# Optimization experiments

Measured on AMD Instinct MI355X. Metric: run time of the kernel, lower is better.

Reference implementation:

```python
import jax, jax.numpy as jnp
import numpy as np

# Spec constants (from init_kwargs)
NUM_ANCHORS = 5
NUM_CLASSES = 80
FM_H = 19
FM_W = 19
MAX_OBJECT = 50
NOOBJECT_SCALE = 1.0
OBJECT_SCALE = 5.0
BACKGROUND_THRESHOLD = 0.6
COORD_SCALE = 1.0
CLASS_SCALE = 1.0


def _iou_cwh(a, b):
    """IoU for boxes in (cx, cy, w, h) format; broadcasts over leading dims.
    Matches bbox_iou(..., x1y1x2y2=False) in the torch repo (0 when no overlap)."""
    ax1, ax2 = a[..., 0] - a[..., 2] * 0.5, a[..., 0] + a[..., 2] * 0.5
    ay1, ay2 = a[..., 1] - a[..., 3] * 0.5, a[..., 1] + a[..., 3] * 0.5
    bx1, bx2 = b[..., 0] - b[..., 2] * 0.5, b[..., 0] + b[..., 2] * 0.5
    by1, by2 = b[..., 1] - b[..., 3] * 0.5, b[..., 1] + b[..., 3] * 0.5
    uw = jnp.maximum(ax2, bx2) - jnp.minimum(ax1, bx1)
    uh = jnp.maximum(ay2, by2) - jnp.minimum(ay1, by1)
    cw = a[..., 2] + b[..., 2] - uw
    ch = a[..., 3] + b[..., 3] - uh
    inter = jnp.where((cw > 0) & (ch > 0), cw * ch, 0.0)
    union = a[..., 2] * a[..., 3] + b[..., 2] * b[..., 3] - inter
    return inter / jnp.maximum(union, 1e-12)


def setup_inputs() -> dict:
    key = jax.random.key(0)
    k1, k2, k3, k4, k5 = jax.random.split(key, 5)
    B, A, C, H, W, T = 64, NUM_ANCHORS, NUM_CLASSES, FM_H, FM_W, MAX_OBJECT
    output = jax.random.normal(k1, (B, A * (5 + C), H, W), jnp.float32) * 0.5
    # targets: per object (class, cx, cy, w, h), normalized to [0,1]; list ends at first cx == 0
    cls_t = jax.random.randint(k2, (B, T), 0, C).astype(jnp.float32)
    xy = jax.random.uniform(k3, (B, T, 2), jnp.float32, minval=0.1, maxval=0.9)
    wh = jax.random.uniform(k4, (B, T, 2), jnp.float32, minval=0.05, maxval=0.4)
    nvalid = jax.random.randint(k5, (B,), 1, T + 1)
    valid = (jnp.arange(T)[None, :] < nvalid[:, None]).astype(jnp.float32)
    tgt = jnp.concatenate([cls_t[..., None], xy, wh], axis=-1) * valid[..., None]
    target = tgt.reshape(B, T * 5)
    anchors = jnp.array([[1.3221, 1.73145], [3.19275, 4.00944], [5.05587, 8.09892],
                         [9.47112, 4.84053], [11.2364, 10.0071]], jnp.float32)
    return {"output": output, "target": target, "anchors": anchors}


def reference(output, target, anchors):
    B = output.shape[0]
    A, C, H, W, T = NUM_ANCHORS, NUM_CLASSES, FM_H, FM_W, MAX_OBJECT
    out = output.reshape(B, A, 5 + C, H, W)
    x = jax.nn.sigmoid(out[:, :, 0])
    y = jax.nn.sigmoid(out[:, :, 1])
    w = out[:, :, 2]
    h = out[:, :, 3]
    conf = jax.nn.sigmoid(out[:, :, 4])
    cls_logits = jnp.transpose(out[:, :, 5:], (0, 1, 3, 4, 2))  # [B,A,H,W,C]

    # decoded predicted boxes in grid units (detached for target building, as in torch)
    px = x + jnp.arange(W, dtype=x.dtype)[None, None, None, :]
    py = y + jnp.arange(H, dtype=x.dtype)[None, None, :, None]
    pw = jnp.exp(w) * anchors[None, :, 0, None, None]
    ph = jnp.exp(h) * anchors[None, :, 1, None, None]
    pred = jax.lax.stop_gradient(jnp.stack([px, py, pw, ph], axis=-1))  # [B,A,H,W,4]

    tgt = target.reshape(B, T, 5)
    cls_t = tgt[..., 0]
    gx = tgt[..., 1] * W
    gy = tgt[..., 2] * H
    gw = tgt[..., 3] * W
    gh = tgt[..., 4] * H
    # break-at-first-zero semantics of the torch loop
    valid = jnp.cumprod((tgt[..., 1] != 0).astype(jnp.int32), axis=1).astype(bool)  # [B,T]

    gt_boxes = jnp.stack([gx, gy, gw, gh], axis=-1)  # [B,T,4]
    # all-pairs pred-vs-gt IoU (replaces per-object python loop)
    pred_flat = pred.reshape(B, A * H * W, 4)
    ious = _iou_cwh(pred_flat[:, :, None, :], gt_boxes[:, None, :, :])  # [B,N,T]
    best_iou = jnp.max(jnp.where(valid[:, None, :], ious, 0.0), axis=-1)  # [B,N]
    conf_mask = jnp.where(best_iou > BACKGROUND_THRESHOLD, 0.0, NOOBJECT_SCALE)
    conf_mask = conf_mask.reshape(B, A, H, W)

    # best anchor per gt: IoU of (w,h) boxes centered at origin
    aw = anchors[:, 0][None, None, :]
    ah = anchors[:, 1][None, None, :]
    inter_a = jnp.minimum(gw[..., None], aw) * jnp.minimum(gh[..., None], ah)
    union_a = gw[..., None] * gh[..., None] + aw * ah - inter_a
    best_n = jnp.argmax(inter_a / jnp.maximum(union_a, 1e-12), axis=-1)  # [B,T]

    gi = jnp.clip(gx.astype(jnp.int32), 0, W - 1)
    gj = jnp.clip(gy.astype(jnp.int32), 0, H - 1)
    bidx = jnp.arange(B)[:, None]
    pred_sel = pred[bidx, best_n, gj, gi]  # [B,T,4]
    iou_obj = _iou_cwh(gt_boxes, pred_sel)  # [B,T]

    N = B * A * H * W
    flat = ((bidx * A + best_n) * H + gj) * W + gi  # [B,T]
    flat = jnp.where(valid, flat, N).reshape(-1)  # invalid -> out of range, dropped

    def scat(vals):
        return jnp.zeros((N,), jnp.float32).at[flat].set(
            vals.reshape(-1), mode="drop").reshape(B, A, H, W)

    coord_mask = scat(jnp.ones_like(gx))
    cls_mask = coord_mask
    conf_mask = conf_mask.reshape(-1).at[flat].set(
        jnp.full((B * T,), OBJECT_SCALE, jnp.float32), mode="drop").reshape(B, A, H, W)
    tx = scat(gx - gi.astype(gx.dtype))
    ty = scat(gy - gj.astype(gy.dtype))
    tw = scat(jnp.log(jnp.maximum(gw, 1e-12) / anchors[best_n, 0]))
    th = scat(jnp.log(jnp.maximum(gh, 1e-12) / anchors[best_n, 1]))
    tconf = scat(iou_obj)
    tcls = scat(cls_t)

    # losses (sum reduction, matching MSELoss/CrossEntropyLoss(size_average=False))
    loss_x = COORD_SCALE * jnp.sum((coord_mask * (x - tx)) ** 2) / 2.0
    loss_y = COORD_SCALE * jnp.sum((coord_mask * (y - ty)) ** 2) / 2.0
    loss_w = COORD_SCALE * jnp.sum((coord_mask * (w - tw)) ** 2) / 2.0
    loss_h = COORD_SCALE * jnp.sum((coord_mask * (h - th)) ** 2) / 2.0
    sq = jnp.sqrt(conf_mask)
    loss_conf = jnp.sum((sq * (conf - tconf)) ** 2) / 2.0
    ce = -jnp.take_along_axis(jax.nn.log_softmax(cls_logits, axis=-1),
                              tcls.astype(jnp.int32)[..., None], axis=-1)[..., 0]
    loss_cls = CLASS_SCALE * jnp.sum(cls_mask * ce)
    return loss_x + loss_y + loss_w + loss_h + loss_conf + loss_cls
```

## Files before the change

kernel.cpp:

```cpp
#include <hip/hip_runtime.h>
#include <math.h>

#define NUM_ANCHORS 5
#define NUM_CLASSES 80
#define FM_H 19
#define FM_W 19
#define MAX_OBJECT 50
#define HW (FM_H * FM_W)
#define CELLS_PER_B (NUM_ANCHORS * HW)
#define CH (5 + NUM_CLASSES)
#define THREADS 512
#define NW (THREADS / 64)
#define BLOCKS_PER_B ((CELLS_PER_B + THREADS - 1) / THREADS)
#define OBJECT_SCALE 5.0f
#define BACKGROUND_THRESHOLD 0.6f

__device__ inline float frcp(float v) { return __builtin_amdgcn_rcpf(v); }
__device__ inline float fsigmoid(float v) { return frcp(1.0f + __expf(-v)); }

__global__ __launch_bounds__(THREADS) void yolov2_main(
    const float* __restrict__ out,
    const float* __restrict__ target,
    const float* __restrict__ anchors,
    float* __restrict__ partial)
{
    const int b    = blockIdx.x / BLOCKS_PER_B;
    const int blk  = blockIdx.x % BLOCKS_PER_B;
    const int cell = blk * THREADS + threadIdx.x;
    const int lane = threadIdx.x & 63;
    const int wid  = threadIdx.x >> 6;

    __shared__ float4 gA[MAX_OBJECT];
    __shared__ float4 gB[MAX_OBJECT];
    __shared__ float4 gT[MAX_OBJECT];
    __shared__ int    gcls[MAX_OBJECT];
    __shared__ int    nv_sh, n_obj;
    __shared__ int    entries[MAX_OBJECT];
    __shared__ float  wsum[NW];

    const bool incell = (cell < CELLS_PER_B);
    const int a    = incell ? (cell / HW) : 0;
    const int hw   = cell - a * HW;
    const int hrow = hw / FM_W;
    const int wcol = hw - hrow * FM_W;

    const float* base = out + ((size_t)(b * NUM_ANCHORS + a) * CH) * HW + hw;
    float ox = 0.f, oy = 0.f, ow = 0.f, oh = 0.f, oc = 0.f;
    if (incell) {
        ox = base[0];
        oy = base[HW];
        ow = base[2 * HW];
        oh = base[3 * HW];
        oc = base[4 * HW];
    }
    const float anc_w = anchors[2 * a];
    const float anc_h = anchors[2 * a + 1];

    if (threadIdx.x == 0) n_obj = 0;

    if (threadIdx.x < 64) {
        const int t = threadIdx.x;
        float f0 = 0.f, f1 = 0.f, f2 = 0.f, f3 = 0.f, f4 = 0.f;
        if (t < MAX_OBJECT) {
            const float* tp = target + (size_t)b * MAX_OBJECT * 5 + t * 5;
            f0 = tp[0]; f1 = tp[1]; f2 = tp[2]; f3 = tp[3]; f4 = tp[4];
        }
        unsigned long long m = __ballot(t < MAX_OBJECT && f1 != 0.0f);
        if (t == 0) nv_sh = __popcll(m);
        if (t < MAX_OBJECT) {
            float gx = f1 * (float)FM_W;
            float gy = f2 * (float)FM_H;
            float gw = f3 * (float)FM_W;
            float gh = f4 * (float)FM_H;
            int bn = 0; float best = -1.0f;
            #pragma unroll
            for (int k = 0; k < NUM_ANCHORS; ++k) {
                float aw = anchors[2 * k], ah = anchors[2 * k + 1];
                float inter = fminf(gw, aw) * fminf(gh, ah);
                float uni = gw * gh + aw * ah - inter;
                float r = inter * frcp(fmaxf(uni, 1e-12f));
                if (r > best) { best = r; bn = k; }
            }
            int gi = (int)gx; gi = gi < 0 ? 0 : (gi > FM_W - 1 ? FM_W - 1 : gi);
            int gj = (int)gy; gj = gj < 0 ? 0 : (gj > FM_H - 1 ? FM_H - 1 : gj);
            int acell = bn * HW + gj * FM_W + gi;
            gA[t] = make_float4(gx - gw * 0.5f, gx + gw * 0.5f,
                                gy - gh * 0.5f, gy + gh * 0.5f);
            gB[t] = make_float4(gw, gh, gw * gh, __int_as_float(acell));
            gT[t] = make_float4(gx - (float)gi, gy - (float)gj,
                                __logf(fmaxf(gw, 1e-12f) * frcp(anchors[2 * bn])),
                                __logf(fmaxf(gh, 1e-12f) * frcp(anchors[2 * bn + 1])));
            gcls[t] = (int)f0;
        }
    }
    __syncthreads();

    const int nv = nv_sh;
    float local = 0.0f;

    if (incell) {
        float x    = fsigmoid(ox);
        float y    = fsigmoid(oy);
        float conf = fsigmoid(oc);
        float px = x + (float)wcol;
        float py = y + (float)hrow;
        float pw = __expf(ow) * anc_w;
        float ph = __expf(oh) * anc_h;
        float ax1 = px - pw * 0.5f, ax2 = px + pw * 0.5f;
        float ay1 = py - ph * 0.5f, ay2 = py + ph * 0.5f;
        float parea = pw * ph;

        bool bg_hit = false;
        int  last_t = -1;
        #pragma unroll 5
        for (int t = 0; t < nv; ++t) {
            float4 A  = gA[t];
            float4 Bv = gB[t];
            float uw = fmaxf(ax2, A.y) - fminf(ax1, A.x);
            float uh = fmaxf(ay2, A.w) - fminf(ay1, A.z);
            float cw  = Bv.x + pw - uw;
            float chh = Bv.y + ph - uh;
            float inter = (cw > 0.f && chh > 0.f) ? cw * chh : 0.f;
            float uni = parea + Bv.z - inter;
            bg_hit = bg_hit || (inter > BACKGROUND_THRESHOLD * uni);
            if (__float_as_int(Bv.w) == cell) last_t = t;
        }

        if (last_t >= 0) {
            float4 A  = gA[last_t];
            float4 Bv = gB[last_t];
            float4 Tt = gT[last_t];
            float uw = fmaxf(ax2, A.y) - fminf(ax1, A.x);
            float uh = fmaxf(ay2, A.w) - fminf(ay1, A.z);
            float cw  = Bv.x + pw - uw;
            float chh = Bv.y + ph - uh;
            float inter = (cw > 0.f && chh > 0.f) ? cw * chh : 0.f;
            float tconf = inter * frcp(fmaxf(parea + Bv.z - inter, 1e-12f));
            float dc = conf - tconf; local += 0.5f * OBJECT_SCALE * dc * dc;
            float dx = x  - Tt.x; local += 0.5f * dx * dx;
            float dy = y  - Tt.y; local += 0.5f * dy * dy;
            float dw = ow - Tt.z; local += 0.5f * dw * dw;
            float dh = oh - Tt.w; local += 0.5f * dh * dh;
            int pos = atomicAdd(&n_obj, 1);
            entries[pos] = cell | (gcls[last_t] << 16);
        } else if (!bg_hit) {
            local += 0.5f * conf * conf;
        }
    }
    __syncthreads();

    const int ne = n_obj;
    const bool ld = (lane < NUM_CLASSES / 2);
    for (int e0 = wid; e0 < ne; e0 += 2 * NW) {
        const int eB = e0 + NW;
        const bool hasB = (eB < ne);

        int pkA    = entries[e0];
        int ecellA = pkA & 0xFFFF;
        int eclsA  = pkA >> 16;
        int eaA  = ecellA / HW;
        const float* clA = out + ((size_t)(b * NUM_ANCHORS + eaA) * CH + 5) * HW
                               + (ecellA - eaA * HW);
        float vA0 = ld ? clA[(2 * lane + 0) * HW] : 0.0f;
        float vA1 = ld ? clA[(2 * lane + 1) * HW] : 0.0f;

        float vB0 = 0.0f, vB1 = 0.0f;
        int eclsB = 0;
        if (hasB) {
            int pkB    = entries[eB];
            int ecellB = pkB & 0xFFFF;
            eclsB      = pkB >> 16;
            int eaB  = ecellB / HW;
            const float* clB = out + ((size_t)(b * NUM_ANCHORS + eaB) * CH + 5) * HW
                                   + (ecellB - eaB * HW);
            vB0 = ld ? clB[(2 * lane + 0) * HW] : 0.0f;
            vB1 = ld ? clB[(2 * lane + 1) * HW] : 0.0f;
        }

        float sA = ld ? (__expf(vA0) + __expf(vA1)) : 0.0f;
        #pragma unroll
        for (int off = 32; off > 0; off >>= 1)
            sA += __shfl_xor(sA, off, 64);
        float tselA = (eclsA & 1) ? vA1 : vA0;
        float tlA = __shfl(tselA, eclsA >> 1, 64);
        if (lane == 0) local += (__logf(sA) - tlA);

        if (hasB) {
            float sB = ld ? (__expf(vB0) + __expf(vB1)) : 0.0f;
            #pragma unroll
            for (int off = 32; off > 0; off >>= 1)
                sB += __shfl_xor(sB, off, 64);
            float tselB = (eclsB & 1) ? vB1 : vB0;
            float tlB = __shfl(tselB, eclsB >> 1, 64);
            if (lane == 0) local += (__logf(sB) - tlB);
        }
    }

    #pragma unroll
    for (int off = 32; off > 0; off >>= 1)
        local += __shfl_down(local, off, 64);
    if (lane == 0) wsum[wid] = local;
    __syncthreads();
    if (threadIdx.x == 0) {
        float tot = 0.0f;
        #pragma unroll
        for (int i = 0; i < NW; ++i) tot += wsum[i];
        partial[blockIdx.x] = tot;
    }
}

__global__ __launch_bounds__(64) void yolov2_reduce(
    const float* __restrict__ partial, int n, float* __restrict__ loss)
{
    const float4* p4 = (const float4*)partial;
    float v = 0.0f;
    for (int i = threadIdx.x; i * 4 < n; i += 64) {
        float4 q = p4[i];
        v += (q.x + q.y) + (q.z + q.w);
    }
    #pragma unroll
    for (int off = 32; off > 0; off >>= 1)
        v += __shfl_down(v, off, 64);
    if (threadIdx.x == 0) loss[0] = v;
}

extern "C" void kernel_launch(void* const* d_in, const int* in_sizes, int n_in,
                              void* d_out, int out_size, void* d_ws, size_t ws_size,
                              hipStream_t stream) {
    const float* out_t   = (const float*)d_in[0];
    const float* target  = (const float*)d_in[1];
    const float* anchors = (const float*)d_in[2];
    float* loss    = (float*)d_out;
    float* partial = (float*)d_ws;

    const int B = in_sizes[1] / (MAX_OBJECT * 5);
    const int nblocks = B * BLOCKS_PER_B;

    yolov2_main<<<dim3(nblocks), dim3(THREADS), 0, stream>>>(out_t, target, anchors, partial);
    yolov2_reduce<<<dim3(1), dim3(64), 0, stream>>>(partial, nblocks, loss);
}
```

Baseline: 16.74 us.

## Fuse final reduction into main kernel via per-block ready flags

Drops the second reduce kernel launch. Each block publishes its partial sum and sets a flag, and block 0 spins until every flag is set, sums the partials and writes the loss, then clears the flags. This saves one kernel launch and its dependency gap. The cost is a spin-wait in block 0, which relies on all blocks being co-resident or scheduled ahead of block 0, and on the flags area in the workspace starting out zeroed.

```diff
diff --git a/kernel.cpp b/kernel.cpp
--- a/kernel.cpp
+++ b/kernel.cpp
@@ -14,6 +14,7 @@
 #define BLOCKS_PER_B ((CELLS_PER_B + THREADS - 1) / THREADS)
 #define OBJECT_SCALE 5.0f
 #define BACKGROUND_THRESHOLD 0.6f
+#define FLAG_MAGIC 0x5AC3D17u
 
 __device__ inline float frcp(float v) { return __builtin_amdgcn_rcpf(v); }
 __device__ inline float fsigmoid(float v) { return frcp(1.0f + __expf(-v)); }
@@ -22,7 +23,9 @@
     const float* __restrict__ out,
     const float* __restrict__ target,
     const float* __restrict__ anchors,
-    float* __restrict__ partial)
+    float* __restrict__ partial,
+    unsigned int* __restrict__ flags,
+    float* __restrict__ loss)
 {
     const int b    = blockIdx.x / BLOCKS_PER_B;
     const int blk  = blockIdx.x % BLOCKS_PER_B;
@@ -205,23 +208,38 @@
         float tot = 0.0f;
         #pragma unroll
         for (int i = 0; i < NW; ++i) tot += wsum[i];
-        partial[blockIdx.x] = tot;
-    }
-}
-
-__global__ __launch_bounds__(64) void yolov2_reduce(
-    const float* __restrict__ partial, int n, float* __restrict__ loss)
-{
-    const float4* p4 = (const float4*)partial;
-    float v = 0.0f;
-    for (int i = threadIdx.x; i * 4 < n; i += 64) {
-        float4 q = p4[i];
-        v += (q.x + q.y) + (q.z + q.w);
-    }
-    #pragma unroll
-    for (int off = 32; off > 0; off >>= 1)
-        v += __shfl_down(v, off, 64);
-    if (threadIdx.x == 0) loss[0] = v;
+        atomicExch(&partial[blockIdx.x], tot);
+    }
+    __threadfence();
+    if (threadIdx.x == 0)
+        atomicExch(&flags[blockIdx.x], FLAG_MAGIC);
+
+    if (blockIdx.x == 0) {
+        const int nb = (int)gridDim.x;
+        if (threadIdx.x < nb) {
+            while (atomicCAS(&flags[threadIdx.x], FLAG_MAGIC, FLAG_MAGIC)
+                   != FLAG_MAGIC) {
+                __builtin_amdgcn_s_sleep(1);
+            }
+        }
+        __syncthreads();
+        float v = 0.0f;
+        if (threadIdx.x < nb)
+            v = atomicAdd(&partial[threadIdx.x], 0.0f);
+        #pragma unroll
+        for (int off = 32; off > 0; off >>= 1)
+            v += __shfl_down(v, off, 64);
+        if (lane == 0) wsum[wid] = v;
+        __syncthreads();
+        if (threadIdx.x == 0) {
+            float tot = 0.0f;
+            #pragma unroll
+            for (int i = 0; i < NW; ++i) tot += wsum[i];
+            loss[0] = tot;
+        }
+        if (threadIdx.x < nb)
+            atomicExch(&flags[threadIdx.x], 0u);
+    }
 }
 
 extern "C" void kernel_launch(void* const* d_in, const int* in_sizes, int n_in,
@@ -230,12 +248,13 @@
     const float* out_t   = (const float*)d_in[0];
     const float* target  = (const float*)d_in[1];
     const float* anchors = (const float*)d_in[2];
-    float* loss    = (float*)d_out;
-    float* partial = (float*)d_ws;
+    float* loss          = (float*)d_out;
+    float* partial       = (float*)d_ws;
+    unsigned int* flags  = (unsigned int*)((char*)d_ws + 4096);
 
     const int B = in_sizes[1] / (MAX_OBJECT * 5);
     const int nblocks = B * BLOCKS_PER_B;
 
-    yolov2_main<<<dim3(nblocks), dim3(THREADS), 0, stream>>>(out_t, target, anchors, partial);
-    yolov2_reduce<<<dim3(1), dim3(64), 0, stream>>>(partial, nblocks, loss);
+    yolov2_main<<<dim3(nblocks), dim3(THREADS), 0, stream>>>(
+        out_t, target, anchors, partial, flags, loss);
 }
```

Result: slower. 49.03 us (+193.0%).

## Fuse reduction into main kernel via atomics and simplify IoU tests

Applied to the files above, without the earlier changes.

Drops the separate reduce kernel launch: each block atomically adds its partial sum straight into the loss, and block 0 zeroes the output first. The background-threshold IoU test is rewritten without a division (1.6*inter > 0.6*(parea+barea)), and the shared gB float4 is replaced with a smaller float2 plus a scalar area. The best-anchor choice now compares cross-multiplied ratios instead of taking reciprocals. The zeroing is racy, since other blocks may run their atomicAdd before block 0 resets the loss, and float atomics make the summation order nondeterministic.

```diff
diff --git a/kernel.cpp b/kernel.cpp
--- a/kernel.cpp
+++ b/kernel.cpp
@@ -13,17 +13,18 @@
 #define NW (THREADS / 64)
 #define BLOCKS_PER_B ((CELLS_PER_B + THREADS - 1) / THREADS)
 #define OBJECT_SCALE 5.0f
-#define BACKGROUND_THRESHOLD 0.6f
 
 __device__ inline float frcp(float v) { return __builtin_amdgcn_rcpf(v); }
 __device__ inline float fsigmoid(float v) { return frcp(1.0f + __expf(-v)); }
 
-__global__ __launch_bounds__(THREADS) void yolov2_main(
+__global__ __launch_bounds__(THREADS) void yolov2_fused(
     const float* __restrict__ out,
     const float* __restrict__ target,
     const float* __restrict__ anchors,
-    float* __restrict__ partial)
+    float* __restrict__ loss)
 {
+    if (blockIdx.x == 0 && threadIdx.x == 0) atomicExch(loss, 0.0f);
+
     const int b    = blockIdx.x / BLOCKS_PER_B;
     const int blk  = blockIdx.x % BLOCKS_PER_B;
     const int cell = blk * THREADS + threadIdx.x;
@@ -31,7 +32,8 @@
     const int wid  = threadIdx.x >> 6;
 
     __shared__ float4 gA[MAX_OBJECT];
-    __shared__ float4 gB[MAX_OBJECT];
+    __shared__ float2 gM[MAX_OBJECT];
+    __shared__ float  gBa[MAX_OBJECT];
     __shared__ float4 gT[MAX_OBJECT];
     __shared__ int    gcls[MAX_OBJECT];
     __shared__ int    nv_sh, n_obj;
@@ -72,21 +74,23 @@
             float gy = f2 * (float)FM_H;
             float gw = f3 * (float)FM_W;
             float gh = f4 * (float)FM_H;
-            int bn = 0; float best = -1.0f;
+            int bn = 0;
+            float bi = -1.0f, bu = 1.0f;
             #pragma unroll
             for (int k = 0; k < NUM_ANCHORS; ++k) {
                 float aw = anchors[2 * k], ah = anchors[2 * k + 1];
-                float inter = fminf(gw, aw) * fminf(gh, ah);
-                float uni = gw * gh + aw * ah - inter;
-                float r = inter * frcp(fmaxf(uni, 1e-12f));
-                if (r > best) { best = r; bn = k; }
+                float ik = fminf(gw, aw) * fminf(gh, ah);
+                float uk = fmaxf(gw * gh + aw * ah - ik, 1e-12f);
+                if (ik * bu > bi * uk) { bi = ik; bu = uk; bn = k; }
             }
             int gi = (int)gx; gi = gi < 0 ? 0 : (gi > FM_W - 1 ? FM_W - 1 : gi);
             int gj = (int)gy; gj = gj < 0 ? 0 : (gj > FM_H - 1 ? FM_H - 1 : gj);
             int acell = bn * HW + gj * FM_W + gi;
+            float barea = gw * gh;
             gA[t] = make_float4(gx - gw * 0.5f, gx + gw * 0.5f,
                                 gy - gh * 0.5f, gy + gh * 0.5f);
-            gB[t] = make_float4(gw, gh, gw * gh, __int_as_float(acell));
+            gM[t] = make_float2(0.6f * barea, __int_as_float(acell));
+            gBa[t] = barea;
             gT[t] = make_float4(gx - (float)gi, gy - (float)gj,
                                 __logf(fmaxf(gw, 1e-12f) * frcp(anchors[2 * bn])),
                                 __logf(fmaxf(gh, 1e-12f) * frcp(anchors[2 * bn + 1])));
@@ -109,33 +113,29 @@
         float ax1 = px - pw * 0.5f, ax2 = px + pw * 0.5f;
         float ay1 = py - ph * 0.5f, ay2 = py + ph * 0.5f;
         float parea = pw * ph;
+        float p6 = 0.6f * parea;
 
         bool bg_hit = false;
         int  last_t = -1;
         #pragma unroll 5
         for (int t = 0; t < nv; ++t) {
-            float4 A  = gA[t];
-            float4 Bv = gB[t];
-            float uw = fmaxf(ax2, A.y) - fminf(ax1, A.x);
-            float uh = fmaxf(ay2, A.w) - fminf(ay1, A.z);
-            float cw  = Bv.x + pw - uw;
-            float chh = Bv.y + ph - uh;
-            float inter = (cw > 0.f && chh > 0.f) ? cw * chh : 0.f;
-            float uni = parea + Bv.z - inter;
-            bg_hit = bg_hit || (inter > BACKGROUND_THRESHOLD * uni);
-            if (__float_as_int(Bv.w) == cell) last_t = t;
+            float4 A = gA[t];
+            float2 M = gM[t];
+            float cwx = fminf(ax2, A.y) - fmaxf(ax1, A.x);
+            float cwy = fminf(ay2, A.w) - fmaxf(ay1, A.z);
+            float inter = cwx * cwy;
+            bg_hit = bg_hit ||
+                     ((cwx > 0.f) && (cwy > 0.f) && (1.6f * inter > p6 + M.x));
+            if (__float_as_int(M.y) == cell) last_t = t;
         }
 
         if (last_t >= 0) {
             float4 A  = gA[last_t];
-            float4 Bv = gB[last_t];
             float4 Tt = gT[last_t];
-            float uw = fmaxf(ax2, A.y) - fminf(ax1, A.x);
-            float uh = fmaxf(ay2, A.w) - fminf(ay1, A.z);
-            float cw  = Bv.x + pw - uw;
-            float chh = Bv.y + ph - uh;
-            float inter = (cw > 0.f && chh > 0.f) ? cw * chh : 0.f;
-            float tconf = inter * frcp(fmaxf(parea + Bv.z - inter, 1e-12f));
+            float cwx = fminf(ax2, A.y) - fmaxf(ax1, A.x);
+            float cwy = fminf(ay2, A.w) - fmaxf(ay1, A.z);
+            float inter = (cwx > 0.f && cwy > 0.f) ? cwx * cwy : 0.f;
+            float tconf = inter * frcp(fmaxf(parea + gBa[last_t] - inter, 1e-12f));
             float dc = conf - tconf; local += 0.5f * OBJECT_SCALE * dc * dc;
             float dx = x  - Tt.x; local += 0.5f * dx * dx;
             float dy = y  - Tt.y; local += 0.5f * dy * dy;
@@ -205,23 +205,8 @@
         float tot = 0.0f;
         #pragma unroll
         for (int i = 0; i < NW; ++i) tot += wsum[i];
-        partial[blockIdx.x] = tot;
-    }
-}
-
-__global__ __launch_bounds__(64) void yolov2_reduce(
-    const float* __restrict__ partial, int n, float* __restrict__ loss)
-{
-    const float4* p4 = (const float4*)partial;
-    float v = 0.0f;
-    for (int i = threadIdx.x; i * 4 < n; i += 64) {
-        float4 q = p4[i];
-        v += (q.x + q.y) + (q.z + q.w);
-    }
-    #pragma unroll
-    for (int off = 32; off > 0; off >>= 1)
-        v += __shfl_down(v, off, 64);
-    if (threadIdx.x == 0) loss[0] = v;
+        atomicAdd(loss, tot);
+    }
 }
 
 extern "C" void kernel_launch(void* const* d_in, const int* in_sizes, int n_in,
@@ -230,12 +215,11 @@
     const float* out_t   = (const float*)d_in[0];
     const float* target  = (const float*)d_in[1];
     const float* anchors = (const float*)d_in[2];
-    float* loss    = (float*)d_out;
-    float* partial = (float*)d_ws;
+    float* loss          = (float*)d_out;
 
     const int B = in_sizes[1] / (MAX_OBJECT * 5);
     const int nblocks = B * BLOCKS_PER_B;
 
-    yolov2_main<<<dim3(nblocks), dim3(THREADS), 0, stream>>>(out_t, target, anchors, partial);
-    yolov2_reduce<<<dim3(1), dim3(64), 0, stream>>>(partial, nblocks, loss);
+    yolov2_fused<<<dim3(nblocks), dim3(THREADS), 0, stream>>>(
+        out_t, target, anchors, loss);
 }
```

After: 16.97 us. Within noise of the previous version (+1.4%).
